# Performance work log

Measured on AMD Instinct MI355X. Metric: run time of the kernel, lower is better.

The kernel has to match this reference:

```python
import jax, jax.numpy as jnp
import numpy as np

N, E, H = 40000, 640000, 128
EPS = 1e-5

def _bn(x, gamma, beta):
    # BatchNorm1d training-mode forward: batch mean / biased variance over axis 0
    mu = jnp.mean(x, axis=0)
    var = jnp.mean((x - mu) ** 2, axis=0)
    return (x - mu) * jax.lax.rsqrt(var + EPS) * gamma + beta


def setup_inputs() -> dict:
    key = jax.random.key(0)
    ks = jax.random.split(key, 12)
    s = 1.0 / np.sqrt(H)
    return {
        "x_feat": jax.random.normal(ks[0], (N, H), jnp.float32),
        "edge_attr": jax.random.normal(ks[1], (E, H), jnp.float32),
        "bases": jax.random.normal(ks[2], (E, H), jnp.float32),
        "src": jax.random.randint(ks[3], (E,), 0, N, jnp.int32),
        "dst": jax.random.randint(ks[4], (E,), 0, N, jnp.int32),
        "W1": jax.random.uniform(ks[5], (H, H), jnp.float32, -s, s),
        "b1": jnp.zeros((H,), jnp.float32),
        "W2": jax.random.uniform(ks[6], (H, H), jnp.float32, -s, s),
        "b2": jnp.zeros((H,), jnp.float32),
        "g1": jnp.ones((H,), jnp.float32),
        "be1": jnp.zeros((H,), jnp.float32),
        "W3": jax.random.uniform(ks[7], (H, H), jnp.float32, -s, s),
        "b3": jnp.zeros((H,), jnp.float32),
        "g2": jnp.ones((H,), jnp.float32),
        "be2": jnpp_zeros if False else jnp.zeros((H,), jnp.float32),
    }


def reference(x_feat, edge_attr, bases, src, dst,
              W1, b1, W2, b2, g1, be1, W3, b3, g2, be2):
    n_nodes = x_feat.shape[0]
    # edge gather-add: pos_e = x[src] + e
    pos_e = x_feat[src] + edge_attr                       # [E, H]
    # pre_ffn (Linear + exact GELU) then elementwise scale by bases
    v = jax.nn.gelu(pos_e @ W1.T + b1, approximate=False) * bases  # [E, H]
    # scatter-sum aggregation to destination nodes
    aggr = jax.ops.segment_sum(v, dst, num_segments=n_nodes)       # [N, H]
    # ffn: Linear -> BN -> GELU -> Linear -> BN -> GELU
    h = _bn(aggr @ W2.T + b2, g1, be1)
    h = jax.nn.gelu(h, approximate=False)
    h = _bn(h @ W3.T + b3, g2, be2)
    return jax.nn.gelu(h, approximate=False)
```

## Files before the change

### kernel.cpp

```cpp
#include <hip/hip_runtime.h>
#include <cmath>

#define H 128
#define EPS 1e-5f

typedef __attribute__((ext_vector_type(8))) __bf16 bf16x8;
typedef __attribute__((ext_vector_type(4))) float f32x4;
typedef __attribute__((ext_vector_type(2))) float f32x2;
typedef __attribute__((ext_vector_type(4))) unsigned short u16x4;
typedef __attribute__((ext_vector_type(8))) unsigned short u16x8;
typedef __attribute__((ext_vector_type(4))) int i32x4;

__device__ __forceinline__ float gelu_fast(float x) {
    float t2 = -1.5957691216057308f * fmaf(0.044715f * x * x, x, x);
    return x * __builtin_amdgcn_rcpf(1.0f + __expf(t2));
}

__device__ __forceinline__ unsigned short f2bfu(float f) {
    __bf16 h = (__bf16)f;
    return __builtin_bit_cast(unsigned short, h);
}

__device__ __forceinline__ float bfu2f(unsigned short u) {
    return __builtin_bit_cast(float, (unsigned)u << 16);
}

__device__ __forceinline__ void gld16(const void* g, void* l) {
    __builtin_amdgcn_global_load_lds(
        (__attribute__((address_space(1))) void*)(g),
        (__attribute__((address_space(3))) void*)(l), 16, 0, 0);
}

__global__ __launch_bounds__(256) void zero_kernel(int* __restrict__ p, int n4)
{
    int i = blockIdx.x * blockDim.x + threadIdx.x;
    const int stride = gridDim.x * blockDim.x;
    i32x4 z = {0, 0, 0, 0};
    for (; i < n4; i += stride)
        reinterpret_cast<i32x4*>(p)[i] = z;
}

__global__ __launch_bounds__(256) void convert_x(const float* __restrict__ x,
                                                 unsigned short* __restrict__ xb,
                                                 long n8)
{
    long i = (long)blockIdx.x * blockDim.x + threadIdx.x;
    const long stride = (long)gridDim.x * blockDim.x;
    for (; i < n8; i += stride) {
        f32x4 a = *reinterpret_cast<const f32x4*>(x + i * 8);
        f32x4 b = *reinterpret_cast<const f32x4*>(x + i * 8 + 4);
        u16x8 o;
#pragma unroll
        for (int j = 0; j < 4; ++j) { o[j] = f2bfu(a[j]); o[j + 4] = f2bfu(b[j]); }
        *reinterpret_cast<u16x8*>(xb + i * 8) = o;
    }
}

__global__ __launch_bounds__(256) void hist_kernel(const int* __restrict__ dst,
                                                   int* __restrict__ cnt, int E)
{
    int i = blockIdx.x * blockDim.x + threadIdx.x;
    const int stride = gridDim.x * blockDim.x;
    for (; i < E; i += stride) atomicAdd(&cnt[dst[i]], 1);
}

__global__ __launch_bounds__(256) void scan_p1(const int* __restrict__ cnt,
                                               int* __restrict__ otmp,
                                               int* __restrict__ bsum, int Nn)
{
    __shared__ int sh[256];
    const int t = threadIdx.x;
    const int idx = blockIdx.x * 256 + t;
    int v = idx < Nn ? cnt[idx] : 0;
    sh[t] = v;
    __syncthreads();
    for (int d = 1; d < 256; d <<= 1) {
        int u = (t >= d) ? sh[t - d] : 0;
        __syncthreads();
        sh[t] += u;
        __syncthreads();
    }
    if (idx < Nn) otmp[idx] = sh[t] - v;
    if (t == 255) bsum[blockIdx.x] = sh[t];
}

__global__ __launch_bounds__(256) void scan_p2(const int* __restrict__ bsum,
                                               int* __restrict__ boff, int nb,
                                               int* __restrict__ offs, int Nn, int E)
{
    __shared__ int sh[256];
    const int t = threadIdx.x;
    int v = t < nb ? bsum[t] : 0;
    sh[t] = v;
    __syncthreads();
    for (int d = 1; d < 256; d <<= 1) {
        int u = (t >= d) ? sh[t - d] : 0;
        __syncthreads();
        sh[t] += u;
        __syncthreads();
    }
    if (t < nb) boff[t] = sh[t] - v;
    if (t == 0) offs[Nn] = E;
}

__global__ __launch_bounds__(256) void scan_p3(const int* __restrict__ otmp,
                                               const int* __restrict__ boff,
                                               int* __restrict__ offs, int Nn)
{
    const int idx = blockIdx.x * 256 + threadIdx.x;
    if (idx < Nn) offs[idx] = otmp[idx] + boff[blockIdx.x];
}

__global__ __launch_bounds__(256) void scatter_perm(const int* __restrict__ dst,
                                                    const int* __restrict__ offs,
                                                    int* __restrict__ cur2,
                                                    int* __restrict__ perm,
                                                    int* __restrict__ dsts, int E)
{
    int i = blockIdx.x * blockDim.x + threadIdx.x;
    const int stride = gridDim.x * blockDim.x;
    for (; i < E; i += stride) {
        int n = dst[i];
        int p = offs[n] + atomicAdd(&cur2[n], 1);
        perm[p] = i;
        dsts[p] = n;
    }
}

__global__ __launch_bounds__(256, 2) void edge_aggr(
    const unsigned short* __restrict__ xbf, const float* __restrict__ ea,
    const float* __restrict__ bases, const int* __restrict__ src,
    const int* __restrict__ perm, const int* __restrict__ dsts,
    const float* __restrict__ W1, const float* __restrict__ b1,
    float* __restrict__ aggr, int E)
{
    __shared__ __align__(16) float ealds[64 * 128];
    __shared__ __align__(16) float blds[64 * 128];
    __shared__ __align__(16) unsigned short xlds[64 * 128];

    const int tid = threadIdx.x;
    const int w = tid >> 6, l = tid & 63, lg = l >> 4, lr = l & 15;

    bf16x8 wf[2][4];
    f32x4 b1v[2];
#pragma unroll
    for (int ni = 0; ni < 2; ++ni) {
        int row = w * 32 + ni * 16 + lr;
#pragma unroll
        for (int kk = 0; kk < 4; ++kk) {
            const float* p = W1 + row * H + kk * 32 + lg * 8;
            u16x8 tt;
#pragma unroll
            for (int i = 0; i < 8; ++i) tt[i] = f2bfu(p[i]);
            wf[ni][kk] = __builtin_bit_cast(bf16x8, tt);
        }
        b1v[ni] = *reinterpret_cast<const f32x4*>(b1 + w * 32 + ni * 16 + lg * 4);
    }

    const int e0 = blockIdx.x * 64;
    int ic = e0 + l;
    ic = ic < E ? ic : E - 1;
    const int el_reg = perm[ic];
    const int nd_reg = dsts[ic];
    const int sr_reg = src[el_reg];

#pragma unroll
    for (int j = 0; j < 8; ++j) {
        const int r = (w << 4) + (j << 1) + (l >> 5);
        const int e = __shfl(el_reg, r);
        const int cs = (l & 31) ^ (r & 7);
        const int rowbase = (((w << 4) + (j << 1)) << 7);
        gld16(ea + (long)e * H + cs * 4, &ealds[rowbase]);
        gld16(bases + (long)e * H + cs * 4, &blds[rowbase]);
    }

#pragma unroll
    for (int j = 0; j < 4; ++j) {
        const int r = (w << 4) + (j << 2) + (l >> 4);
        const int s = __shfl(sr_reg, r);
        const int cs = (l & 15) ^ (r & 7);
        const int rowbase = (((w << 4) + (j << 2)) << 7);
        gld16(xbf + (long)s * H + cs * 8, &xlds[rowbase]);
    }
    __syncthreads();

    const int col0base = w * 32 + lg * 4;
#pragma unroll
    for (int s = 0; s < 4; ++s) {
        const int arow = s * 16 + lr;
        const int fswz = arow & 7;

        bf16x8 af[4];
#pragma unroll
        for (int kk = 0; kk < 4; ++kk) {
            const int cc = kk * 8 + lg * 2;
            f32x4 elo = *reinterpret_cast<const f32x4*>(&ealds[arow * 128 + ((cc ^ fswz) << 2)]);
            f32x4 ehi = *reinterpret_cast<const f32x4*>(&ealds[arow * 128 + (((cc + 1) ^ fswz) << 2)]);
            u16x8 xv = *reinterpret_cast<const u16x8*>(&xlds[arow * 128 + (((kk * 4 + lg) ^ fswz) << 3)]);
            u16x8 o;
#pragma unroll
            for (int r = 0; r < 4; ++r) {
                o[r]     = f2bfu(elo[r] + bfu2f(xv[r]));
                o[r + 4] = f2bfu(ehi[r] + bfu2f(xv[r + 4]));
            }
            af[kk] = __builtin_bit_cast(bf16x8, o);
        }

        const int es = e0 + arow;
        const bool ok = es < E;
        const int nd = __shfl(nd_reg, arow);
        const int ndp = __shfl(nd_reg, arow - 1);
        const bool head = ok && (lr == 0 || nd != ndp);

#pragma unroll
        for (int ni = 0; ni < 2; ++ni) {
            f32x4 a4 = b1v[ni];
#pragma unroll
            for (int kk = 0; kk < 4; ++kk)
                a4 = __builtin_amdgcn_mfma_f32_16x16x32_bf16(wf[ni][kk], af[kk], a4, 0, 0, 0);

            const int col0 = col0base + ni * 16;
            const int bcc = col0 >> 2;
            f32x4 bq = *reinterpret_cast<const f32x4*>(&blds[arow * 128 + ((bcc ^ fswz) << 2)]);
            f32x4 v;
#pragma unroll
            for (int r = 0; r < 4; ++r)
                v[r] = ok ? gelu_fast(a4[r]) * bq[r] : 0.f;

#pragma unroll
            for (int d = 1; d < 16; d <<= 1) {
                f32x4 vn;
#pragma unroll
                for (int r = 0; r < 4; ++r) vn[r] = __shfl_down(v[r], d);
                int ndn = __shfl_down(nd, d);
                bool take = (lr + d < 16) && (ndn == nd);
#pragma unroll
                for (int r = 0; r < 4; ++r) v[r] += take ? vn[r] : 0.f;
            }

            if (head) {
                float* dstp = aggr + (long)nd * H + col0;
#pragma unroll
                for (int r = 0; r < 4; ++r) atomicAdd(&dstp[r], v[r]);
            }
        }
    }
}

template <bool PRE>
__global__ __launch_bounds__(256) void node_gemm(
    const float* __restrict__ A, const float* __restrict__ W,
    const float* __restrict__ bias, const float* __restrict__ scl,
    const float* __restrict__ shf, float* __restrict__ Y,
    float* __restrict__ csum, float* __restrict__ cssq, int Nn)
{
    __shared__ __align__(16) unsigned short alds[64 * 128];

    const int tid = threadIdx.x;
    const int w = tid >> 6, l = tid & 63, lg = l >> 4, lr = l & 15;
    const int er = tid >> 2, q = tid & 3;
    const int r0 = blockIdx.x * 64;

    bf16x8 bf[2][4];
    float bv[2];
#pragma unroll
    for (int n = 0; n < 2; ++n) {
        int row = w * 32 + n * 16 + lr;
        bv[n] = bias[row];
#pragma unroll
        for (int kk = 0; kk < 4; ++kk) {
            const float* p = W + row * H + kk * 32 + lg * 8;
            u16x8 t;
#pragma unroll
            for (int i = 0; i < 8; ++i) t[i] = f2bfu(p[i]);
            bf[n][kk] = __builtin_bit_cast(bf16x8, t);
        }
    }

    {
        int rr = r0 + er;
        int rc = rr < Nn ? rr : Nn - 1;
        const f32x4* pa = reinterpret_cast<const f32x4*>(A + (long)rc * H + q * 32);
        const int swz = (er & 7) << 3;
#pragma unroll
        for (int i = 0; i < 8; ++i) {
            f32x4 v = pa[i];
            if constexpr (PRE) {
                f32x4 sc = *reinterpret_cast<const f32x4*>(scl + q * 32 + i * 4);
                f32x4 sh = *reinterpret_cast<const f32x4*>(shf + q * 32 + i * 4);
#pragma unroll
                for (int c = 0; c < 4; ++c) v[c] = gelu_fast(v[c] * sc[c] + sh[c]);
            }
            u16x4 o;
            o[0] = f2bfu(v[0]);
            o[1] = f2bfu(v[1]);
            o[2] = f2bfu(v[2]);
            o[3] = f2bfu(v[3]);
            int col = q * 32 + i * 4;
            *reinterpret_cast<u16x4*>(&alds[er * 128 + (col ^ swz)]) = o;
        }
    }
    __syncthreads();

    float ps[2] = {0.f, 0.f}, ps2[2] = {0.f, 0.f};
#pragma unroll
    for (int m = 0; m < 4; ++m) {
        const int arow = m * 16 + lr;
        const int aswz = (arow & 7) << 3;
        bf16x8 af[4];
#pragma unroll
        for (int kk = 0; kk < 4; ++kk)
            af[kk] = __builtin_bit_cast(bf16x8,
                *reinterpret_cast<const u16x8*>(&alds[arow * 128 + ((kk * 32 + lg * 8) ^ aswz)]));
#pragma unroll
        for (int n = 0; n < 2; ++n) {
            f32x4 a4 = {0.f, 0.f, 0.f, 0.f};
#pragma unroll
            for (int kk = 0; kk < 4; ++kk)
                a4 = __builtin_amdgcn_mfma_f32_16x16x32_bf16(af[kk], bf[n][kk], a4, 0, 0, 0);
            const int j = w * 32 + n * 16 + lr;
#pragma unroll
            for (int r = 0; r < 4; ++r) {
                int rr = r0 + m * 16 + lg * 4 + r;
                if (rr < Nn) {
                    float z = a4[r] + bv[n];
                    Y[(long)rr * H + j] = z;
                    ps[n] += z;
                    ps2[n] += z * z;
                }
            }
        }
    }
#pragma unroll
    for (int n = 0; n < 2; ++n) {
        float s = ps[n];
        s += __shfl_xor(s, 16);
        s += __shfl_xor(s, 32);
        float s2 = ps2[n];
        s2 += __shfl_xor(s2, 16);
        s2 += __shfl_xor(s2, 32);
        if (lg == 0) {
            int j = w * 32 + n * 16 + lr;
            atomicAdd(&csum[j], s);
            atomicAdd(&cssq[j], s2);
        }
    }
}

__global__ void finalize_bn(const float* __restrict__ csum, const float* __restrict__ cssq,
                            const float* __restrict__ g, const float* __restrict__ be,
                            float* __restrict__ scl, float* __restrict__ shf, float invN)
{
    int j = threadIdx.x;
    float mu = csum[j] * invN;
    float var = fmaxf(cssq[j] * invN - mu * mu, 0.f);
    float s = g[j] * rsqrtf(var + EPS);
    scl[j] = s;
    shf[j] = be[j] - mu * s;
}

__global__ __launch_bounds__(256) void final_gelu(
    const float* __restrict__ Y2, const float* __restrict__ scl,
    const float* __restrict__ shf, float* __restrict__ out, long n4)
{
    long i = (long)blockIdx.x * blockDim.x + threadIdx.x;
    const long stride = (long)gridDim.x * blockDim.x;
    for (; i < n4; i += stride) {
        f32x4 v = reinterpret_cast<const f32x4*>(Y2)[i];
        int c4 = (int)(i & 31);
        f32x4 sc = reinterpret_cast<const f32x4*>(scl)[c4];
        f32x4 sh = reinterpret_cast<const f32x4*>(shf)[c4];
        f32x4 o;
#pragma unroll
        for (int c = 0; c < 4; ++c) o[c] = gelu_fast(v[c] * sc[c] + sh[c]);
        reinterpret_cast<f32x4*>(out)[i] = o;
    }
}

extern "C" void kernel_launch(void* const* d_in, const int* in_sizes, int n_in,
                              void* d_out, int out_size, void* d_ws, size_t ws_size,
                              hipStream_t stream) {
    const float* x     = (const float*)d_in[0];
    const float* ea    = (const float*)d_in[1];
    const float* bases = (const float*)d_in[2];
    const int*   src   = (const int*)d_in[3];
    const int*   dst   = (const int*)d_in[4];
    const float* W1    = (const float*)d_in[5];
    const float* b1    = (const float*)d_in[6];
    const float* W2    = (const float*)d_in[7];
    const float* b2    = (const float*)d_in[8];
    const float* g1    = (const float*)d_in[9];
    const float* be1   = (const float*)d_in[10];
    const float* W3    = (const float*)d_in[11];
    const float* b3    = (const float*)d_in[12];
    const float* g2    = (const float*)d_in[13];
    const float* be2   = (const float*)d_in[14];

    const int N = in_sizes[0] / H;
    const int E = in_sizes[1] / H;

    float* ws    = (float*)d_ws;
    float* aggr  = ws;
    float* y1    = aggr + (size_t)N * H;
    float* stats = y1 + (size_t)N * H;
    float* sum1 = stats,        *ss1 = stats + 128;
    float* sum2 = stats + 256,  *ss2 = stats + 384;
    float* scl1 = stats + 512,  *shf1 = stats + 640;
    float* scl2 = stats + 768,  *shf2 = stats + 896;
    int* cnt  = (int*)(stats + 1024);
    int* cnt2 = cnt + N;
    int* perm = cnt2 + N;
    int* dsts = perm + E;
    int* offs = dsts + E;
    int* otmp = offs + N + 1;
    int* bsum = otmp + N;
    int* boff = bsum + 256;
    unsigned short* xbf = (unsigned short*)(((uintptr_t)(boff + 256) + 4095) & ~(uintptr_t)4095);

    const int zn4 = (1024 + 2 * N + 3) / 4;
    zero_kernel<<<128, 256, 0, stream>>>((int*)stats, zn4);
    zero_kernel<<<1024, 256, 0, stream>>>((int*)aggr, N * H / 4);

    convert_x<<<2048, 256, 0, stream>>>(x, xbf, (long)N * H / 8);

    const int nsb = (N + 255) / 256;
    hist_kernel<<<2048, 256, 0, stream>>>(dst, cnt, E);
    scan_p1<<<nsb, 256, 0, stream>>>(cnt, otmp, bsum, N);
    scan_p2<<<1, 256, 0, stream>>>(bsum, boff, nsb, offs, N, E);
    scan_p3<<<nsb, 256, 0, stream>>>(otmp, boff, offs, N);
    scatter_perm<<<2048, 256, 0, stream>>>(dst, offs, cnt2, perm, dsts, E);

    edge_aggr<<<(E + 63) / 64, 256, 0, stream>>>(xbf, ea, bases, src, perm, dsts,
                                                 W1, b1, aggr, E);

    const int nblk = (N + 63) / 64;
    node_gemm<false><<<nblk, 256, 0, stream>>>(aggr, W2, b2, nullptr, nullptr, y1, sum1, ss1, N);
    finalize_bn<<<1, 128, 0, stream>>>(sum1, ss1, g1, be1, scl1, shf1, 1.0f / (float)N);
    node_gemm<true><<<nblk, 256, 0, stream>>>(y1, W3, b3, scl1, shf1, aggr, sum2, ss2, N);
    finalize_bn<<<1, 128, 0, stream>>>(sum2, ss2, g2, be2, scl2, shf2, 1.0f / (float)N);

    long n4 = (long)N * H / 4;
    final_gelu<<<2048, 256, 0, stream>>>(aggr, scl2, shf2, (float*)d_out, n4);
}
```

Baseline: 393.6 us.

## Make edge_aggr persistent with double-buffered LDS staging and direct x gathers

The edge aggregation kernel becomes persistent, running on a fixed grid of 512 blocks that loop over 64-edge tiles. Edge-attribute and basis rows for the next tile are staged asynchronously into a second LDS buffer while the current tile is computed, and per-tile metadata is prefetched two tiles ahead. The bf16 x rows are now read directly from global memory into registers instead of being staged in LDS, which frees LDS for the double buffer. The aim is to hide global gather latency and remove per-block launch and W1 setup costs. In exchange, LDS use per block doubles (128 KB), which likely limits occupancy to one block per CU, and the direct x loads may stall the compute.

Result: slower. 491.9 us (+25.0%).

```diff
diff --git a/kernel.cpp b/kernel.cpp
--- a/kernel.cpp
+++ b/kernel.cpp
@@ -127,16 +127,15 @@
     }
 }
 
-__global__ __launch_bounds__(256, 2) void edge_aggr(
+__global__ __launch_bounds__(256) void edge_aggr(
     const unsigned short* __restrict__ xbf, const float* __restrict__ ea,
     const float* __restrict__ bases, const int* __restrict__ src,
     const int* __restrict__ perm, const int* __restrict__ dsts,
     const float* __restrict__ W1, const float* __restrict__ b1,
     float* __restrict__ aggr, int E)
 {
-    __shared__ __align__(16) float ealds[64 * 128];
-    __shared__ __align__(16) float blds[64 * 128];
-    __shared__ __align__(16) unsigned short xlds[64 * 128];
+    __shared__ __align__(16) float ealds[2][64 * 128];
+    __shared__ __align__(16) float blds[2][64 * 128];
 
     const int tid = threadIdx.x;
     const int w = tid >> 6, l = tid & 63, lg = l >> 4, lr = l & 15;
@@ -157,94 +156,125 @@
         b1v[ni] = *reinterpret_cast<const f32x4*>(b1 + w * 32 + ni * 16 + lg * 4);
     }
 
-    const int e0 = blockIdx.x * 64;
-    int ic = e0 + l;
-    ic = ic < E ? ic : E - 1;
-    const int el_reg = perm[ic];
-    const int nd_reg = dsts[ic];
-    const int sr_reg = src[el_reg];
-
-#pragma unroll
-    for (int j = 0; j < 8; ++j) {
-        const int r = (w << 4) + (j << 1) + (l >> 5);
-        const int e = __shfl(el_reg, r);
-        const int cs = (l & 31) ^ (r & 7);
-        const int rowbase = (((w << 4) + (j << 1)) << 7);
-        gld16(ea + (long)e * H + cs * 4, &ealds[rowbase]);
-        gld16(bases + (long)e * H + cs * 4, &blds[rowbase]);
-    }
-
-#pragma unroll
-    for (int j = 0; j < 4; ++j) {
-        const int r = (w << 4) + (j << 2) + (l >> 4);
-        const int s = __shfl(sr_reg, r);
-        const int cs = (l & 15) ^ (r & 7);
-        const int rowbase = (((w << 4) + (j << 2)) << 7);
-        gld16(xbf + (long)s * H + cs * 8, &xlds[rowbase]);
-    }
+    const int ntiles = (E + 63) / 64;
+    int t = blockIdx.x;
+    if (t >= ntiles) return;
+    const int tstride = gridDim.x;
+
+#define LOADMETA(ELV, NDV, SRV, TT)                                          \
+    {                                                                        \
+        int ic_ = (TT) * 64 + l;                                             \
+        ic_ = ic_ < E ? ic_ : E - 1;                                         \
+        ELV = perm[ic_];                                                     \
+        NDV = dsts[ic_];                                                     \
+        SRV = src[ELV];                                                      \
+    }
+
+#define STAGE(BB, ELV)                                                       \
+    {                                                                        \
+        _Pragma("unroll")                                                    \
+        for (int j = 0; j < 8; ++j) {                                        \
+            const int r_ = (w << 4) + (j << 1) + (l >> 5);                   \
+            const int e_ = __shfl(ELV, r_);                                  \
+            const int cs_ = (l & 31) ^ (r_ & 7);                             \
+            const int rb_ = (((w << 4) + (j << 1)) << 7);                    \
+            gld16(ea + (long)e_ * H + cs_ * 4, &ealds[BB][rb_]);             \
+            gld16(bases + (long)e_ * H + cs_ * 4, &blds[BB][rb_]);           \
+        }                                                                    \
+    }
+
+    int el0, nd0, sr0, el1, nd1, sr1, el2, nd2, sr2;
+    LOADMETA(el0, nd0, sr0, t);
+    STAGE(0, el0);
+    LOADMETA(el1, nd1, sr1, t + tstride);
     __syncthreads();
 
+    int cur = 0;
     const int col0base = w * 32 + lg * 4;
-#pragma unroll
-    for (int s = 0; s < 4; ++s) {
-        const int arow = s * 16 + lr;
-        const int fswz = arow & 7;
-
-        bf16x8 af[4];
-#pragma unroll
-        for (int kk = 0; kk < 4; ++kk) {
-            const int cc = kk * 8 + lg * 2;
-            f32x4 elo = *reinterpret_cast<const f32x4*>(&ealds[arow * 128 + ((cc ^ fswz) << 2)]);
-            f32x4 ehi = *reinterpret_cast<const f32x4*>(&ealds[arow * 128 + (((cc + 1) ^ fswz) << 2)]);
-            u16x8 xv = *reinterpret_cast<const u16x8*>(&xlds[arow * 128 + (((kk * 4 + lg) ^ fswz) << 3)]);
-            u16x8 o;
-#pragma unroll
-            for (int r = 0; r < 4; ++r) {
-                o[r]     = f2bfu(elo[r] + bfu2f(xv[r]));
-                o[r + 4] = f2bfu(ehi[r] + bfu2f(xv[r + 4]));
+    while (true) {
+        const bool more = (t + tstride) < ntiles;
+        if (more) STAGE(cur ^ 1, el1);
+        LOADMETA(el2, nd2, sr2, t + 2 * tstride);
+
+        const int e0 = t * 64;
+#pragma unroll
+        for (int s = 0; s < 4; ++s) {
+            const int arow = s * 16 + lr;
+            const int fswz = arow & 7;
+
+            const long xrow = (long)__shfl(sr0, arow) * H;
+            u16x8 xv[4];
+#pragma unroll
+            for (int kk = 0; kk < 4; ++kk)
+                xv[kk] = *reinterpret_cast<const u16x8*>(xbf + xrow + kk * 32 + lg * 8);
+
+            bf16x8 af[4];
+#pragma unroll
+            for (int kk = 0; kk < 4; ++kk) {
+                const int cc = kk * 8 + lg * 2;
+                f32x4 elo = *reinterpret_cast<const f32x4*>(
+                    &ealds[cur][arow * 128 + ((cc ^ fswz) << 2)]);
+                f32x4 ehi = *reinterpret_cast<const f32x4*>(
+                    &ealds[cur][arow * 128 + (((cc + 1) ^ fswz) << 2)]);
+                u16x8 o;
+#pragma unroll
+                for (int r = 0; r < 4; ++r) {
+                    o[r]     = f2bfu(elo[r] + bfu2f(xv[kk][r]));
+                    o[r + 4] = f2bfu(ehi[r] + bfu2f(xv[kk][r + 4]));
+                }
+                af[kk] = __builtin_bit_cast(bf16x8, o);
             }
-            af[kk] = __builtin_bit_cast(bf16x8, o);
-        }
-
-        const int es = e0 + arow;
-        const bool ok = es < E;
-        const int nd = __shfl(nd_reg, arow);
-        const int ndp = __shfl(nd_reg, arow - 1);
-        const bool head = ok && (lr == 0 || nd != ndp);
-
-#pragma unroll
-        for (int ni = 0; ni < 2; ++ni) {
-            f32x4 a4 = b1v[ni];
-#pragma unroll
-            for (int kk = 0; kk < 4; ++kk)
-                a4 = __builtin_amdgcn_mfma_f32_16x16x32_bf16(wf[ni][kk], af[kk], a4, 0, 0, 0);
-
-            const int col0 = col0base + ni * 16;
-            const int bcc = col0 >> 2;
-            f32x4 bq = *reinterpret_cast<const f32x4*>(&blds[arow * 128 + ((bcc ^ fswz) << 2)]);
-            f32x4 v;
-#pragma unroll
-            for (int r = 0; r < 4; ++r)
-                v[r] = ok ? gelu_fast(a4[r]) * bq[r] : 0.f;
-
-#pragma unroll
-            for (int d = 1; d < 16; d <<= 1) {
-                f32x4 vn;
-#pragma unroll
-                for (int r = 0; r < 4; ++r) vn[r] = __shfl_down(v[r], d);
-                int ndn = __shfl_down(nd, d);
-                bool take = (lr + d < 16) && (ndn == nd);
-#pragma unroll
-                for (int r = 0; r < 4; ++r) v[r] += take ? vn[r] : 0.f;
+
+            const int es = e0 + arow;
+            const bool ok = es < E;
+            const int nd = __shfl(nd0, arow);
+            const int ndp = __shfl(nd0, arow - 1);
+            const bool head = ok && (lr == 0 || nd != ndp);
+
+#pragma unroll
+            for (int ni = 0; ni < 2; ++ni) {
+                f32x4 a4 = b1v[ni];
+#pragma unroll
+                for (int kk = 0; kk < 4; ++kk)
+                    a4 = __builtin_amdgcn_mfma_f32_16x16x32_bf16(wf[ni][kk], af[kk], a4, 0, 0, 0);
+
+                const int col0 = col0base + ni * 16;
+                const int bcc = col0 >> 2;
+                f32x4 bq = *reinterpret_cast<const f32x4*>(
+                    &blds[cur][arow * 128 + ((bcc ^ fswz) << 2)]);
+                f32x4 v;
+#pragma unroll
+                for (int r = 0; r < 4; ++r)
+                    v[r] = ok ? gelu_fast(a4[r]) * bq[r] : 0.f;
+
+#pragma unroll
+                for (int d = 1; d < 16; d <<= 1) {
+                    f32x4 vn;
+#pragma unroll
+                    for (int r = 0; r < 4; ++r) vn[r] = __shfl_down(v[r], d);
+                    int ndn = __shfl_down(nd, d);
+                    bool take = (lr + d < 16) && (ndn == nd);
+#pragma unroll
+                    for (int r = 0; r < 4; ++r) v[r] += take ? vn[r] : 0.f;
+                }
+
+                if (head) {
+                    float* dstp = aggr + (long)nd * H + col0;
+#pragma unroll
+                    for (int r = 0; r < 4; ++r) atomicAdd(&dstp[r], v[r]);
+                }
             }
-
-            if (head) {
-                float* dstp = aggr + (long)nd * H + col0;
-#pragma unroll
-                for (int r = 0; r < 4; ++r) atomicAdd(&dstp[r], v[r]);
-            }
-        }
-    }
+        }
+
+        if (!more) break;
+        __syncthreads();
+        el0 = el1; nd0 = nd1; sr0 = sr1;
+        el1 = el2; nd1 = nd2; sr1 = sr2;
+        cur ^= 1;
+        t += tstride;
+    }
+#undef LOADMETA
+#undef STAGE
 }
 
 template <bool PRE>
@@ -430,8 +460,8 @@
     scan_p3<<<nsb, 256, 0, stream>>>(otmp, boff, offs, N);
     scatter_perm<<<2048, 256, 0, stream>>>(dst, offs, cnt2, perm, dsts, E);
 
-    edge_aggr<<<(E + 63) / 64, 256, 0, stream>>>(xbf, ea, bases, src, perm, dsts,
-                                                 W1, b1, aggr, E);
+    edge_aggr<<<512, 256, 0, stream>>>(xbf, ea, bases, src, perm, dsts,
+                                       W1, b1, aggr, E);
 
     const int nblk = (N + 63) / 64;
     node_gemm<false><<<nblk, 256, 0, stream>>>(aggr, W2, b2, nullptr, nullptr, y1, sum1, ss1, N);
```
